# Optimization experiments

Measured on AMD Instinct MI355X. Metric: run time of the kernel, lower is better.

The kernel has to match this reference:

```python
import jax, jax.numpy as jnp
import numpy as np

N, DIM, OUT, E = 10000, 256, 256, 320000


def setup_inputs() -> dict:
    key = jax.random.key(0)
    ks = jax.random.split(key, 10)
    def w(k, shape):
        fan_in = shape[0]
        return jax.random.normal(k, shape, jnp.float32) * (fan_in ** -0.5)
    return {
        "v_c": jax.random.normal(ks[0], (N, DIM), jnp.float32),
        # row-normalized-ish random adjacency weights so A @ v stays O(1)
        "A": jax.random.uniform(ks[1], (N, N), jnp.float32) * (2.0 / N),
        "src": jax.random.randint(ks[2], (E,), 0, N, jnp.int32),
        "dst": jax.random.randint(ks[3], (E,), 0, N, jnp.int32),
        # ResidualBlock params: lin1 (dim -> 2dim), lin2 (2dim -> dim)
        "W1": w(ks[4], (DIM, 2 * DIM)), "b1": jnp.zeros((2 * DIM,), jnp.float32),
        "W2": w(ks[5], (2 * DIM, DIM)), "b2": jnp.zeros((DIM,), jnp.float32),
        # LatticeMP_Block lin1 / lin2 (dim -> out_dim)
        "Wl1": w(ks[6], (DIM, OUT)), "bl1": jnp.zeros((OUT,), jnp.float32),
        "Wl2": w(ks[7], (DIM, OUT)), "bl2": jnp.zeros((OUT,), jnp.float32),
    }


def reference(v_c, A, src, dst, W1, b1, W2, b2, Wl1, bl1, Wl2, bl2):
    # ResidualBlock: relu(h + lin2(relu(lin1(h))))
    h1 = jnp.maximum(v_c @ W1 + b1, 0.0) @ W2 + b2          # [N, DIM]
    v = jnp.maximum(v_c + h1, 0.0)                           # [N, DIM]
    # relu(lin1(v)) + relu(lin2(A @ v))
    v = jnp.maximum(v @ Wl1 + bl1, 0.0) + jnp.maximum((A @ v) @ Wl2 + bl2, 0.0)  # [N, OUT]
    # DGL update_all(copy_u, sum): h_N[d] = sum_{(s,d) in E} v[s]
    h_N = jax.ops.segment_sum(v[src], dst, num_segments=N)   # [N, OUT]
    return h_N + v
```

## Files before the change

kernel.cpp:

```cpp
#include <hip/hip_runtime.h>
#include <stdint.h>

#define NN 10000
#define DIMV 256
#define HID 512
#define NEDGE 320000
#define SPLIT 6
#define KCH 1664
#define NKT 313
#define APL 2112
#define ABUF 8448
#define BOFF 16896
#define LDSZ 49664

typedef __attribute__((ext_vector_type(8))) short bf16x8;
typedef __attribute__((ext_vector_type(4))) float f32x4;
typedef __attribute__((ext_vector_type(4))) unsigned short u16x4;
typedef __attribute__((ext_vector_type(2))) unsigned int u32x2;

__device__ __forceinline__ unsigned short f2bf(float f) {
  union { float f; unsigned int u; } c; c.f = f;
  return (unsigned short)((c.u + 0x7FFFu + ((c.u >> 16) & 1u)) >> 16);
}
__device__ __forceinline__ float bf2f(unsigned short h) {
  union { unsigned int u; float f; } c; c.u = ((unsigned int)h) << 16;
  return c.f;
}

__device__ __forceinline__ bf16x8 bzero8() {
  bf16x8 r;
#pragma unroll
  for (int i = 0; i < 8; ++i) r[i] = 0;
  return r;
}

__device__ __forceinline__ bf16x8 pack8(const float* x) {
  bf16x8 r;
#pragma unroll
  for (int i = 0; i < 8; ++i) r[i] = (short)f2bf(x[i]);
  return r;
}

__device__ __forceinline__ u32x2 cvt4v(const f32x4 a) {
  u32x2 r;
  asm("v_cvt_pk_bf16_f32 %0, %1, %2" : "=v"(r[0]) : "v"(a[0]), "v"(a[1]));
  asm("v_cvt_pk_bf16_f32 %0, %1, %2" : "=v"(r[1]) : "v"(a[2]), "v"(a[3]));
  return r;
}

typedef __attribute__((address_space(1))) unsigned int gu32;
typedef __attribute__((address_space(3))) unsigned int lu32;
__device__ __forceinline__ void glds16(const void* g, void* l) {
  __builtin_amdgcn_global_load_lds((const gu32*)g, (lu32*)l, 16, 0, 0);
}

__global__ void k_conv(const float* __restrict__ W1, const float* __restrict__ W2,
                       const float* __restrict__ Wl1, const float* __restrict__ Wl2,
                       unsigned short* __restrict__ W1T, unsigned short* __restrict__ W2T,
                       unsigned short* __restrict__ Wl1T, unsigned short* __restrict__ Wl2T,
                       unsigned short* __restrict__ vB, int* __restrict__ counts) {
  int i = blockIdx.x * 256 + threadIdx.x;
  if (i < 131072) {
    { int k = i >> 9, o = i & 511; W1T[o * 256 + k] = f2bf(W1[i]); }
    { int k = i >> 8, o = i & 255; W2T[o * 512 + k] = f2bf(W2[i]); }
    if (i < 65536) {
      int k = i >> 8, o = i & 255;
      Wl1T[o * 256 + k] = f2bf(Wl1[i]);
      Wl2T[o * 256 + k] = f2bf(Wl2[i]);
    }
    if (i < 4096) {
      int c = i >> 4, kk = 16 + (i & 15);
      int g = kk >> 3;
      int byte = c * 64 + ((g ^ ((c >> 1) & 3)) << 4) + (kk & 7) * 2;
      *(unsigned short*)((char*)vB + (size_t)312 * 16384 + byte) = 0;
    }
    if (i < NN) counts[i] = 0;
  }
}

__launch_bounds__(256, 2)
__global__ void k_mlp(const float* __restrict__ vc,
                      const unsigned short* __restrict__ W1T, const float* __restrict__ b1,
                      const unsigned short* __restrict__ W2T, const float* __restrict__ b2,
                      unsigned short* __restrict__ v_rm, unsigned short* __restrict__ vB,
                      const int* __restrict__ dst, int* __restrict__ counts) {
  if (blockIdx.x >= 313) {
    const int e0 = (blockIdx.x - 313) * 256 + threadIdx.x;
    for (int e = e0; e < NEDGE; e += 40 * 256) atomicAdd(&counts[dst[e]], 1);
    return;
  }
  __shared__ __align__(16) char sm[65536];
  const int t = threadIdx.x;
  const int lane = t & 63, wid = t >> 6;
  const int wr = wid & 1, wc = wid >> 1;
  const int r0 = blockIdx.x * 32;

  {
    const int row = t >> 3, grow = r0 + row;
#pragma unroll
    for (int q = 0; q < 4; ++q) {
      const int slot = (t & 7) * 4 + q;
      float buf[8] = {0.f, 0.f, 0.f, 0.f, 0.f, 0.f, 0.f, 0.f};
      if (grow < NN) {
        const float4 x0 = *(const float4*)(vc + (size_t)grow * DIMV + slot * 8);
        const float4 x1 = *(const float4*)(vc + (size_t)grow * DIMV + slot * 8 + 4);
        buf[0] = x0.x; buf[1] = x0.y; buf[2] = x0.z; buf[3] = x0.w;
        buf[4] = x1.x; buf[5] = x1.y; buf[6] = x1.z; buf[7] = x1.w;
      }
      *(bf16x8*)(sm + row * 512 + ((slot ^ (row & 7)) * 16)) = pack8(buf);
    }
  }

  f32x4 acc1[16];
#pragma unroll
  for (int i = 0; i < 16; ++i) acc1[i] = (f32x4){0.f, 0.f, 0.f, 0.f};

  for (int step = 0; step < 8; ++step) {
    __syncthreads();
#pragma unroll
    for (int rr = 0; rr < 2; ++rr) {
      const int c = t + rr * 256;
      const unsigned short* srcp = W1T + c * 256 + step * 32;
#pragma unroll
      for (int q = 0; q < 4; ++q) {
        bf16x8 w = *(const bf16x8*)(srcp + q * 8);
        *(bf16x8*)(sm + 16384 + c * 64 + ((q ^ ((c >> 1) & 3)) * 16)) = w;
      }
    }
    __syncthreads();
    const int arow = 16 * wr + (lane & 15);
    const int aslot = step * 4 + (lane >> 4);
    const bf16x8 af = *(const bf16x8*)(sm + arow * 512 + ((aslot ^ (arow & 7)) * 16));
#pragma unroll
    for (int ct = 0; ct < 16; ++ct) {
      const int c = 256 * wc + 16 * ct + (lane & 15);
      const bf16x8 bfr =
          *(const bf16x8*)(sm + 16384 + c * 64 + ((((lane >> 4)) ^ ((c >> 1) & 3)) * 16));
      acc1[ct] = __builtin_amdgcn_mfma_f32_16x16x32_bf16(af, bfr, acc1[ct], 0, 0, 0);
    }
  }
  __syncthreads();
#pragma unroll
  for (int ct = 0; ct < 16; ++ct) {
    const int c = 256 * wc + 16 * ct + (lane & 15);
    const float bb = b1[c];
#pragma unroll
    for (int r = 0; r < 4; ++r) {
      const int row = 16 * wr + (lane >> 4) * 4 + r;
      float v = fmaxf(acc1[ct][r] + bb, 0.f);
      const int slot = c >> 3;
      *(unsigned short*)(sm + 16384 + row * 1024 + ((slot ^ (row & 7)) * 16) + (c & 7) * 2) =
          f2bf(v);
    }
  }

  f32x4 acc2[8];
#pragma unroll
  for (int i = 0; i < 8; ++i) acc2[i] = (f32x4){0.f, 0.f, 0.f, 0.f};

  for (int step = 0; step < 16; ++step) {
    __syncthreads();
    {
      const int c = t;
      const unsigned short* srcp = W2T + c * 512 + step * 32;
#pragma unroll
      for (int q = 0; q < 4; ++q) {
        bf16x8 w = *(const bf16x8*)(srcp + q * 8);
        *(bf16x8*)(sm + 49152 + c * 64 + ((q ^ ((c >> 1) & 3)) * 16)) = w;
      }
    }
    __syncthreads();
    const int arow = 16 * wr + (lane & 15);
    const int aslot = step * 4 + (lane >> 4);
    const bf16x8 af = *(const bf16x8*)(sm + 16384 + arow * 1024 + ((aslot ^ (arow & 7)) * 16));
#pragma unroll
    for (int ct = 0; ct < 8; ++ct) {
      const int c = 128 * wc + 16 * ct + (lane & 15);
      const bf16x8 bfr =
          *(const bf16x8*)(sm + 49152 + c * 64 + ((((lane >> 4)) ^ ((c >> 1) & 3)) * 16));
      acc2[ct] = __builtin_amdgcn_mfma_f32_16x16x32_bf16(af, bfr, acc2[ct], 0, 0, 0);
    }
  }

  const int growbase = r0 + 16 * wr + (lane >> 4) * 4;
  if (growbase < NN) {
#pragma unroll
    for (int ct = 0; ct < 8; ++ct) {
      const int c = 128 * wc + 16 * ct + (lane & 15);
      const float bb = b2[c];
      u16x4 pk;
#pragma unroll
      for (int r = 0; r < 4; ++r) {
        const int grow = growbase + r;
        float v = acc2[ct][r] + bb + vc[(size_t)grow * DIMV + c];
        v = fmaxf(v, 0.f);
        const unsigned short hv = f2bf(v);
        v_rm[(size_t)grow * DIMV + c] = hv;
        pk[r] = hv;
      }
      const int tile = growbase >> 5, kk0 = growbase & 31;
      const int g = kk0 >> 3;
      const int byte = c * 64 + ((g ^ ((c >> 1) & 3)) << 4) + (kk0 & 7) * 2;
      *(u16x4*)((char*)vB + (size_t)tile * 16384 + byte) = pk;
    }
  }
}

__launch_bounds__(512, 4)
__global__ void k_av(const float* __restrict__ A, const unsigned short* __restrict__ vB,
                     unsigned short* __restrict__ avpb,
                     const int* __restrict__ counts, int* __restrict__ offsets,
                     int* __restrict__ cursor) {
  __shared__ __align__(16) char sm[LDSZ];
  const int t = threadIdx.x, lane = t & 63, wid = t >> 6;

  if (blockIdx.x >= 474) {
    int* wred = (int*)sm;
    int carry = 0;
    for (int base = 0; base < NN; base += 512) {
      const int i = base + t;
      const int x = (i < NN) ? counts[i] : 0;
      int v = x;
#pragma unroll
      for (int d = 1; d < 64; d <<= 1) {
        int y = __shfl_up(v, d);
        if (lane >= d) v += y;
      }
      if (lane == 63) wred[wid] = v;
      __syncthreads();
      if (t < 8) {
        int sv = wred[t];
#pragma unroll
        for (int d = 1; d < 8; d <<= 1) {
          int y = __shfl_up(sv, d);
          if (t >= d) sv += y;
        }
        wred[t] = sv;
      }
      __syncthreads();
      const int excl = carry + (wid ? wred[wid - 1] : 0) + v - x;
      if (i < NN) { offsets[i] = excl; cursor[i] = excl; }
      carry += wred[7];
      __syncthreads();
    }
    if (t == 0) offsets[NN] = carry;
    return;
  }

  const int wr = wid >> 2, wc = wid & 3;

  const int orig = blockIdx.x;
  const int xcd = orig & 7, idx = orig >> 3;
  const int g = (xcd < 2) ? xcd * 60 + idx : 120 + (xcd - 2) * 59 + idx;
  const int s = g / 79;
  const int xb = g - s * 79;
  const int r0 = xb * 128;
  const int kbase = s * KCH;
  const int tile0 = s * 52;
  const int nst = (s == SPLIT - 1) ? 53 : 52;
  unsigned short* outp = avpb + (size_t)s * NN * DIMV;

  const int srow = t >> 3, sQ = t & 7;
  const float* ap0 = A + (size_t)min(r0 + srow, NN - 1) * NN;
  const float* ap1 = A + (size_t)min(r0 + 64 + srow, NN - 1) * NN;
  const int wbase = (sQ >> 1) * APL + (sQ & 1) * 8;
  const int w0 = wbase + srow * 16;
  const int w1 = wbase + (64 + srow) * 16;

  f32x4 aR0, aR1, bR0, bR1;

#define AISSUE_A(ST)                                          \
  do {                                                        \
    int kq = min(kbase + (ST)*32 + sQ * 4, 9996);             \
    aR0 = *(const f32x4*)(ap0 + kq);                          \
    aR1 = *(const f32x4*)(ap1 + kq);                          \
  } while (0)
#define AISSUE_B(ST)                                          \
  do {                                                        \
    int kq = min(kbase + (ST)*32 + sQ * 4, 9996);             \
    bR0 = *(const f32x4*)(ap0 + kq);                          \
    bR1 = *(const f32x4*)(ap1 + kq);                          \
  } while (0)
#define AWRITE_A(BUF)                                         \
  do {                                                        \
    char* wb = sm + (BUF)*ABUF;                               \
    *(u32x2*)(wb + w0) = cvt4v(aR0);                          \
    *(u32x2*)(wb + w1) = cvt4v(aR1);                          \
  } while (0)
#define AWRITE_B(BUF)                                         \
  do {                                                        \
    char* wb = sm + (BUF)*ABUF;                               \
    *(u32x2*)(wb + w0) = cvt4v(bR0);                          \
    *(u32x2*)(wb + w1) = cvt4v(bR1);                          \
  } while (0)

#define BSTAGE(BUF, TILE)                                                     \
  do {                                                                        \
    char* lb = sm + BOFF + (BUF)*16384 + wid * 1024;                          \
    const char* gp = (const char*)vB + (size_t)(TILE)*16384 + wid * 1024 +    \
                     lane * 16;                                               \
    glds16(gp, lb);                                                           \
    glds16(gp + 8192, lb + 8192);                                             \
  } while (0)

  f32x4 acc[4][4];
#pragma unroll
  for (int i = 0; i < 4; ++i)
#pragma unroll
    for (int j = 0; j < 4; ++j) acc[i][j] = (f32x4){0.f, 0.f, 0.f, 0.f};

  const int rbase = (lane >> 4) * APL + (wr * 64 + (lane & 15)) * 16;
  int boff[4];
#pragma unroll
  for (int ct = 0; ct < 4; ++ct) {
    const int col = wc * 64 + ct * 16 + (lane & 15);
    boff[ct] = col * 64 + (((lane >> 4) ^ ((col >> 1) & 3)) << 4);
  }

#define COMPUTE(CUR)                                                               \
  do {                                                                            \
    const char* ab = sm + (CUR)*ABUF;                                             \
    const char* bb = sm + BOFF + (CUR)*16384;                                     \
    const bf16x8 af0 = *(const bf16x8*)(ab + rbase);                              \
    const bf16x8 af1 = *(const bf16x8*)(ab + rbase + 256);                        \
    const bf16x8 af2 = *(const bf16x8*)(ab + rbase + 512);                        \
    const bf16x8 af3 = *(const bf16x8*)(ab + rbase + 768);                        \
    _Pragma("unroll") for (int ct = 0; ct < 4; ++ct) {                            \
      const bf16x8 bfr = *(const bf16x8*)(bb + boff[ct]);                         \
      acc[0][ct] = __builtin_amdgcn_mfma_f32_16x16x32_bf16(af0, bfr, acc[0][ct], 0, 0, 0); \
      acc[1][ct] = __builtin_amdgcn_mfma_f32_16x16x32_bf16(af1, bfr, acc[1][ct], 0, 0, 0); \
      acc[2][ct] = __builtin_amdgcn_mfma_f32_16x16x32_bf16(af2, bfr, acc[2][ct], 0, 0, 0); \
      acc[3][ct] = __builtin_amdgcn_mfma_f32_16x16x32_bf16(af3, bfr, acc[3][ct], 0, 0, 0); \
    }                                                                             \
  } while (0)

  AISSUE_A(0);
  AWRITE_A(0);
  BSTAGE(0, tile0);
  AISSUE_B(1);
  __builtin_amdgcn_sched_barrier(0);
  asm volatile("s_waitcnt lgkmcnt(0)" ::: "memory");
  asm volatile("s_waitcnt vmcnt(2)" ::: "memory");
  __builtin_amdgcn_sched_barrier(0);
  __builtin_amdgcn_s_barrier();

  int cur = 0;
  for (int st = 0; st < nst; ++st) {
    const bool more = (st + 1 < nst);
    const bool more2 = (st + 2 < nst);
    if (more) BSTAGE(cur ^ 1, tile0 + st + 1);
    if (more2) {
      if ((st & 1) == 0) AISSUE_A(st + 2); else AISSUE_B(st + 2);
    }
    COMPUTE(cur);
    if (more) {
      if ((st & 1) == 0) AWRITE_B(cur ^ 1); else AWRITE_A(cur ^ 1);
    }
    __builtin_amdgcn_sched_barrier(0);
    asm volatile("s_waitcnt lgkmcnt(0)" ::: "memory");
    if (more2) asm volatile("s_waitcnt vmcnt(2)" ::: "memory");
    else       asm volatile("s_waitcnt vmcnt(0)" ::: "memory");
    __builtin_amdgcn_sched_barrier(0);
    __builtin_amdgcn_s_barrier();
    cur ^= 1;
  }
#undef AISSUE_A
#undef AISSUE_B
#undef AWRITE_A
#undef AWRITE_B
#undef BSTAGE
#undef COMPUTE

#pragma unroll
  for (int rt = 0; rt < 4; ++rt) {
    const int gb = r0 + wr * 64 + rt * 16 + (lane >> 4) * 4;
    if (gb < NN) {
#pragma unroll
      for (int ct = 0; ct < 4; ++ct) {
        const int col = wc * 64 + ct * 16 + (lane & 15);
#pragma unroll
        for (int r = 0; r < 4; ++r)
          outp[(size_t)(gb + r) * DIMV + col] = f2bf(acc[rt][ct][r]);
      }
    }
  }
}

__launch_bounds__(256, 2)
__global__ void k_out(const unsigned short* __restrict__ v_rm,
                      const unsigned short* __restrict__ avpb,
                      const unsigned short* __restrict__ Wl1T, const float* __restrict__ bl1,
                      const unsigned short* __restrict__ Wl2T, const float* __restrict__ bl2,
                      unsigned short* __restrict__ v2b, float* __restrict__ outb,
                      const int* __restrict__ src, const int* __restrict__ dst,
                      int* __restrict__ cursor, int* __restrict__ srcbuf) {
  if (blockIdx.x >= 313) {
    const int e0 = (blockIdx.x - 313) * 256 + threadIdx.x;
    for (int e = e0; e < NEDGE; e += 40 * 256) {
      const int pos = atomicAdd(&cursor[dst[e]], 1);
      srcbuf[pos] = src[e];
    }
    return;
  }
  __shared__ __align__(16) char sm[65536];
  const int t = threadIdx.x, lane = t & 63, wid = t >> 6;
  const int wr = wid & 1, wc = wid >> 1;
  const int r0 = blockIdx.x * 32;

  {
    const int row = t >> 3, grow = r0 + row;
#pragma unroll
    for (int q = 0; q < 4; ++q) {
      const int slot = (t & 7) * 4 + q;
      bf16x8 w = (grow < NN) ? *(const bf16x8*)(v_rm + (size_t)grow * DIMV + slot * 8) : bzero8();
      *(bf16x8*)(sm + row * 512 + ((slot ^ (row & 7)) * 16)) = w;
    }
#pragma unroll
    for (int q = 0; q < 4; ++q) {
      const int slot = (t & 7) * 4 + q;
      float buf[8] = {0.f, 0.f, 0.f, 0.f, 0.f, 0.f, 0.f, 0.f};
      if (grow < NN) {
#pragma unroll
        for (int p = 0; p < SPLIT; ++p) {
          const bf16x8 a =
              *(const bf16x8*)(avpb + (size_t)p * NN * DIMV + (size_t)grow * DIMV + slot * 8);
#pragma unroll
          for (int z = 0; z < 8; ++z) buf[z] += bf2f((unsigned short)a[z]);
        }
      }
      *(bf16x8*)(sm + 16384 + row * 512 + ((slot ^ (row & 7)) * 16)) = pack8(buf);
    }
  }

  f32x4 acc1[8], acc2[8];
#pragma unroll
  for (int i = 0; i < 8; ++i) {
    acc1[i] = (f32x4){0.f, 0.f, 0.f, 0.f};
    acc2[i] = (f32x4){0.f, 0.f, 0.f, 0.f};
  }

  for (int step = 0; step < 8; ++step) {
    __syncthreads();
    {
      const int c = t;
      const unsigned short* s1 = Wl1T + c * 256 + step * 32;
      const unsigned short* s2 = Wl2T + c * 256 + step * 32;
#pragma unroll
      for (int q = 0; q < 4; ++q) {
        const int ps = (q ^ ((c >> 1) & 3)) * 16;
        *(bf16x8*)(sm + 32768 + c * 64 + ps) = *(const bf16x8*)(s1 + q * 8);
        *(bf16x8*)(sm + 49152 + c * 64 + ps) = *(const bf16x8*)(s2 + q * 8);
      }
    }
    __syncthreads();
    const int arow = 16 * wr + (lane & 15);
    const int aslot = step * 4 + (lane >> 4);
    const bf16x8 a1 = *(const bf16x8*)(sm + arow * 512 + ((aslot ^ (arow & 7)) * 16));
    const bf16x8 a2 = *(const bf16x8*)(sm + 16384 + arow * 512 + ((aslot ^ (arow & 7)) * 16));
#pragma unroll
    for (int ct = 0; ct < 8; ++ct) {
      const int c = 128 * wc + 16 * ct + (lane & 15);
      const int bs = (((lane >> 4)) ^ ((c >> 1) & 3)) * 16;
      acc1[ct] = __builtin_amdgcn_mfma_f32_16x16x32_bf16(
          a1, *(const bf16x8*)(sm + 32768 + c * 64 + bs), acc1[ct], 0, 0, 0);
      acc2[ct] = __builtin_amdgcn_mfma_f32_16x16x32_bf16(
          a2, *(const bf16x8*)(sm + 49152 + c * 64 + bs), acc2[ct], 0, 0, 0);
    }
  }

  const int growbase = r0 + 16 * wr + (lane >> 4) * 4;
  if (growbase < NN) {
#pragma unroll
    for (int ct = 0; ct < 8; ++ct) {
      const int c = 128 * wc + 16 * ct + (lane & 15);
      const float u1 = bl1[c], u2 = bl2[c];
#pragma unroll
      for (int r = 0; r < 4; ++r) {
        const float x = fmaxf(acc1[ct][r] + u1, 0.f) + fmaxf(acc2[ct][r] + u2, 0.f);
        v2b[(size_t)(growbase + r) * DIMV + c] = f2bf(x);
        outb[(size_t)(growbase + r) * DIMV + c] = x;
      }
    }
  }
}

__launch_bounds__(256)
__global__ void k_gather(const unsigned short* __restrict__ v2b,
                         const int* __restrict__ offsets,
                         const int* __restrict__ srcbuf, float* __restrict__ outb) {
  const int n = (blockIdx.x * 256 + threadIdx.x) >> 6;
  if (n >= NN) return;
  const int lane = threadIdx.x & 63;
  const int beg = offsets[n], end = offsets[n + 1];
  float4 a0 = {0.f, 0.f, 0.f, 0.f}, a1 = a0, a2 = a0, a3 = a0;
  float4 a4 = a0, a5 = a0, a6 = a0, a7 = a0;
  int j = beg;
  for (; j + 8 <= end; j += 8) {
    const int s0 = srcbuf[j], s1 = srcbuf[j + 1], s2 = srcbuf[j + 2], s3 = srcbuf[j + 3];
    const int s4 = srcbuf[j + 4], s5 = srcbuf[j + 5], s6 = srcbuf[j + 6], s7 = srcbuf[j + 7];
    const u16x4 x0 = *(const u16x4*)(v2b + (size_t)s0 * DIMV + lane * 4);
    const u16x4 x1 = *(const u16x4*)(v2b + (size_t)s1 * DIMV + lane * 4);
    const u16x4 x2 = *(const u16x4*)(v2b + (size_t)s2 * DIMV + lane * 4);
    const u16x4 x3 = *(const u16x4*)(v2b + (size_t)s3 * DIMV + lane * 4);
    const u16x4 x4 = *(const u16x4*)(v2b + (size_t)s4 * DIMV + lane * 4);
    const u16x4 x5 = *(const u16x4*)(v2b + (size_t)s5 * DIMV + lane * 4);
    const u16x4 x6 = *(const u16x4*)(v2b + (size_t)s6 * DIMV + lane * 4);
    const u16x4 x7 = *(const u16x4*)(v2b + (size_t)s7 * DIMV + lane * 4);
    a0.x += bf2f(x0[0]); a0.y += bf2f(x0[1]); a0.z += bf2f(x0[2]); a0.w += bf2f(x0[3]);
    a1.x += bf2f(x1[0]); a1.y += bf2f(x1[1]); a1.z += bf2f(x1[2]); a1.w += bf2f(x1[3]);
    a2.x += bf2f(x2[0]); a2.y += bf2f(x2[1]); a2.z += bf2f(x2[2]); a2.w += bf2f(x2[3]);
    a3.x += bf2f(x3[0]); a3.y += bf2f(x3[1]); a3.z += bf2f(x3[2]); a3.w += bf2f(x3[3]);
    a4.x += bf2f(x4[0]); a4.y += bf2f(x4[1]); a4.z += bf2f(x4[2]); a4.w += bf2f(x4[3]);
    a5.x += bf2f(x5[0]); a5.y += bf2f(x5[1]); a5.z += bf2f(x5[2]); a5.w += bf2f(x5[3]);
    a6.x += bf2f(x6[0]); a6.y += bf2f(x6[1]); a6.z += bf2f(x6[2]); a6.w += bf2f(x6[3]);
    a7.x += bf2f(x7[0]); a7.y += bf2f(x7[1]); a7.z += bf2f(x7[2]); a7.w += bf2f(x7[3]);
  }
  for (; j < end; ++j) {
    const int s0 = srcbuf[j];
    const u16x4 x0 = *(const u16x4*)(v2b + (size_t)s0 * DIMV + lane * 4);
    a0.x += bf2f(x0[0]); a0.y += bf2f(x0[1]); a0.z += bf2f(x0[2]); a0.w += bf2f(x0[3]);
  }
  a0.x += a1.x + a2.x + a3.x + a4.x + a5.x + a6.x + a7.x;
  a0.y += a1.y + a2.y + a3.y + a4.y + a5.y + a6.y + a7.y;
  a0.z += a1.z + a2.z + a3.z + a4.z + a5.z + a6.z + a7.z;
  a0.w += a1.w + a2.w + a3.w + a4.w + a5.w + a6.w + a7.w;
  float* o = outb + (size_t)n * DIMV + lane * 4;
  float4 cur = *(const float4*)o;
  cur.x += a0.x; cur.y += a0.y; cur.z += a0.z; cur.w += a0.w;
  *(float4*)o = cur;
}

extern "C" void kernel_launch(void* const* d_in, const int* in_sizes, int n_in,
                              void* d_out, int out_size, void* d_ws, size_t ws_size,
                              hipStream_t stream) {
  const float* vc  = (const float*)d_in[0];
  const float* A   = (const float*)d_in[1];
  const int*   src = (const int*)d_in[2];
  const int*   dst = (const int*)d_in[3];
  const float* W1  = (const float*)d_in[4];
  const float* b1  = (const float*)d_in[5];
  const float* W2  = (const float*)d_in[6];
  const float* b2  = (const float*)d_in[7];
  const float* Wl1 = (const float*)d_in[8];
  const float* bl1 = (const float*)d_in[9];
  const float* Wl2 = (const float*)d_in[10];
  const float* bl2 = (const float*)d_in[11];
  float* outb = (float*)d_out;
  char* ws = (char*)d_ws;

  unsigned short* W1T  = (unsigned short*)(ws + 0);
  unsigned short* W2T  = (unsigned short*)(ws + 262144);
  unsigned short* Wl1T = (unsigned short*)(ws + 524288);
  unsigned short* Wl2T = (unsigned short*)(ws + 655360);
  unsigned short* vB   = (unsigned short*)(ws + 786432);
  unsigned short* v_rm = (unsigned short*)(ws + 5914624);
  int* counts  = (int*)(ws + 11034624);
  int* offsets = (int*)(ws + 11075584);
  int* cursor  = (int*)(ws + 11116544);
  int* srcbuf  = (int*)(ws + 11157504);
  unsigned short* avpb = (unsigned short*)(ws + 12437760);
  unsigned short* v2b  = (unsigned short*)(ws + 43157760);

  hipLaunchKernelGGL(k_conv, dim3(512), dim3(256), 0, stream,
                     W1, W2, Wl1, Wl2, W1T, W2T, Wl1T, Wl2T, vB, counts);
  hipLaunchKernelGGL(k_mlp, dim3(353), dim3(256), 0, stream,
                     vc, W1T, b1, W2T, b2, v_rm, vB, dst, counts);
  hipLaunchKernelGGL(k_av, dim3(475), dim3(512), 0, stream,
                     A, vB, avpb, counts, offsets, cursor);
  hipLaunchKernelGGL(k_out, dim3(353), dim3(256), 0, stream,
                     v_rm, avpb, Wl1T, bl1, Wl2T, bl2, v2b, outb,
                     src, dst, cursor, srcbuf);
  hipLaunchKernelGGL(k_gather, dim3((NN * 64 + 255) / 256), dim3(256), 0, stream,
                     v2b, offsets, srcbuf, outb);
}
```

Baseline: 239.5 us.

## Load two A K-steps per issue with 16-byte writes and pad K tiles

The A@v kernel now loads 8 floats per thread per row, covering two K-steps at once. It writes them to LDS as single 16-byte stores into a four-slot A buffer, where it previously issued 4-float loads every step. The K range is padded to 324 tiles so all six splits run an equal 54 steps, and the padding region of vB is zeroed. This halves the number of global-load issue points and evens the load across splits. In exchange it uses more LDS, about 67KB against 49KB, which may reduce occupancy, and it does extra padded work.

New measurement: 238.2 us. About the same (-0.5%).

```diff
diff --git a/kernel.cpp b/kernel.cpp
--- a/kernel.cpp
+++ b/kernel.cpp
@@ -6,17 +6,18 @@
 #define HID 512
 #define NEDGE 320000
 #define SPLIT 6
-#define KCH 1664
-#define NKT 313
-#define APL 2112
-#define ABUF 8448
-#define BOFF 16896
-#define LDSZ 49664
+#define KCH 1728
+#define NKTP 324
+#define APL 2144
+#define ABUF 8576
+#define BOFF 34304
+#define LDSZ 67072
 
 typedef __attribute__((ext_vector_type(8))) short bf16x8;
 typedef __attribute__((ext_vector_type(4))) float f32x4;
 typedef __attribute__((ext_vector_type(4))) unsigned short u16x4;
 typedef __attribute__((ext_vector_type(2))) unsigned int u32x2;
+typedef __attribute__((ext_vector_type(4))) unsigned int u32x4;
 
 __device__ __forceinline__ unsigned short f2bf(float f) {
   union { float f; unsigned int u; } c; c.f = f;
@@ -68,11 +69,8 @@
       Wl1T[o * 256 + k] = f2bf(Wl1[i]);
       Wl2T[o * 256 + k] = f2bf(Wl2[i]);
     }
-    if (i < 4096) {
-      int c = i >> 4, kk = 16 + (i & 15);
-      int g = kk >> 3;
-      int byte = c * 64 + ((g ^ ((c >> 1) & 3)) << 4) + (kk & 7) * 2;
-      *(unsigned short*)((char*)vB + (size_t)312 * 16384 + byte) = 0;
+    if (i < 49152) {
+      ((unsigned int*)vB)[1277952 + i] = 0;
     }
     if (i < NN) counts[i] = 0;
   }
@@ -256,42 +254,34 @@
   const int xb = g - s * 79;
   const int r0 = xb * 128;
   const int kbase = s * KCH;
-  const int tile0 = s * 52;
-  const int nst = (s == SPLIT - 1) ? 53 : 52;
+  const int tile0 = s * 54;
+  const int nst = 54;
   unsigned short* outp = avpb + (size_t)s * NN * DIMV;
 
   const int srow = t >> 3, sQ = t & 7;
   const float* ap0 = A + (size_t)min(r0 + srow, NN - 1) * NN;
   const float* ap1 = A + (size_t)min(r0 + 64 + srow, NN - 1) * NN;
-  const int wbase = (sQ >> 1) * APL + (sQ & 1) * 8;
-  const int w0 = wbase + srow * 16;
-  const int w1 = wbase + (64 + srow) * 16;
-
-  f32x4 aR0, aR1, bR0, bR1;
-
-#define AISSUE_A(ST)                                          \
+
+  f32x4 aR0, aR1, aR2, aR3;
+
+#define AISSUE2(ST)                                           \
   do {                                                        \
-    int kq = min(kbase + (ST)*32 + sQ * 4, 9996);             \
+    int kq = min(kbase + (ST)*32 + sQ * 8, 9992);             \
     aR0 = *(const f32x4*)(ap0 + kq);                          \
-    aR1 = *(const f32x4*)(ap1 + kq);                          \
+    aR1 = *(const f32x4*)(ap0 + kq + 4);                      \
+    aR2 = *(const f32x4*)(ap1 + kq);                          \
+    aR3 = *(const f32x4*)(ap1 + kq + 4);                      \
   } while (0)
-#define AISSUE_B(ST)                                          \
+
+#define AWRITE2(PJ)                                           \
   do {                                                        \
-    int kq = min(kbase + (ST)*32 + sQ * 4, 9996);             \
-    bR0 = *(const f32x4*)(ap0 + kq);                          \
-    bR1 = *(const f32x4*)(ap1 + kq);                          \
-  } while (0)
-#define AWRITE_A(BUF)                                         \
-  do {                                                        \
-    char* wb = sm + (BUF)*ABUF;                               \
-    *(u32x2*)(wb + w0) = cvt4v(aR0);                          \
-    *(u32x2*)(wb + w1) = cvt4v(aR1);                          \
-  } while (0)
-#define AWRITE_B(BUF)                                         \
-  do {                                                        \
-    char* wb = sm + (BUF)*ABUF;                               \
-    *(u32x2*)(wb + w0) = cvt4v(bR0);                          \
-    *(u32x2*)(wb + w1) = cvt4v(bR1);                          \
+    char* base_ = sm + (2 * (PJ) + (sQ >> 2)) * ABUF + (sQ & 3) * APL; \
+    u32x2 lo_ = cvt4v(aR0), hi_ = cvt4v(aR1);                 \
+    u32x4 w0_ = {lo_[0], lo_[1], hi_[0], hi_[1]};             \
+    *(u32x4*)(base_ + srow * 16) = w0_;                       \
+    lo_ = cvt4v(aR2); hi_ = cvt4v(aR3);                       \
+    u32x4 w1_ = {lo_[0], lo_[1], hi_[0], hi_[1]};             \
+    *(u32x4*)(base_ + (64 + srow) * 16) = w1_;                \
   } while (0)
 
 #define BSTAGE(BUF, TILE)                                                     \
@@ -317,9 +307,9 @@
     boff[ct] = col * 64 + (((lane >> 4) ^ ((col >> 1) & 3)) << 4);
   }
 
-#define COMPUTE(CUR)                                                               \
+#define COMPUTE(ST, CUR)                                                           \
   do {                                                                            \
-    const char* ab = sm + (CUR)*ABUF;                                             \
+    const char* ab = sm + (2 * (((ST) >> 1) & 1) + ((ST)&1)) * ABUF;              \
     const char* bb = sm + BOFF + (CUR)*16384;                                     \
     const bf16x8 af0 = *(const bf16x8*)(ab + rbase);                              \
     const bf16x8 af1 = *(const bf16x8*)(ab + rbase + 256);                        \
@@ -334,40 +324,33 @@
     }                                                                             \
   } while (0)
 
-  AISSUE_A(0);
-  AWRITE_A(0);
+  AISSUE2(0);
   BSTAGE(0, tile0);
-  AISSUE_B(1);
+  AWRITE2(0);
   __builtin_amdgcn_sched_barrier(0);
   asm volatile("s_waitcnt lgkmcnt(0)" ::: "memory");
-  asm volatile("s_waitcnt vmcnt(2)" ::: "memory");
+  asm volatile("s_waitcnt vmcnt(0)" ::: "memory");
   __builtin_amdgcn_sched_barrier(0);
   __builtin_amdgcn_s_barrier();
 
   int cur = 0;
   for (int st = 0; st < nst; ++st) {
     const bool more = (st + 1 < nst);
-    const bool more2 = (st + 2 < nst);
+    const bool issueA = ((st & 1) == 0) && (st + 2 < nst);
     if (more) BSTAGE(cur ^ 1, tile0 + st + 1);
-    if (more2) {
-      if ((st & 1) == 0) AISSUE_A(st + 2); else AISSUE_B(st + 2);
-    }
-    COMPUTE(cur);
-    if (more) {
-      if ((st & 1) == 0) AWRITE_B(cur ^ 1); else AWRITE_A(cur ^ 1);
-    }
+    if (issueA) AISSUE2(st + 2);
+    COMPUTE(st, cur);
+    if ((st & 1) == 1 && more) AWRITE2(((st + 1) >> 1) & 1);
     __builtin_amdgcn_sched_barrier(0);
     asm volatile("s_waitcnt lgkmcnt(0)" ::: "memory");
-    if (more2) asm volatile("s_waitcnt vmcnt(2)" ::: "memory");
-    else       asm volatile("s_waitcnt vmcnt(0)" ::: "memory");
+    if (issueA) asm volatile("s_waitcnt vmcnt(4)" ::: "memory");
+    else        asm volatile("s_waitcnt vmcnt(0)" ::: "memory");
     __builtin_amdgcn_sched_barrier(0);
     __builtin_amdgcn_s_barrier();
     cur ^= 1;
   }
-#undef AISSUE_A
-#undef AISSUE_B
-#undef AWRITE_A
-#undef AWRITE_B
+#undef AISSUE2
+#undef AWRITE2
 #undef BSTAGE
 #undef COMPUTE
 
@@ -553,13 +536,13 @@
   unsigned short* Wl1T = (unsigned short*)(ws + 524288);
   unsigned short* Wl2T = (unsigned short*)(ws + 655360);
   unsigned short* vB   = (unsigned short*)(ws + 786432);
-  unsigned short* v_rm = (unsigned short*)(ws + 5914624);
-  int* counts  = (int*)(ws + 11034624);
-  int* offsets = (int*)(ws + 11075584);
-  int* cursor  = (int*)(ws + 11116544);
-  int* srcbuf  = (int*)(ws + 11157504);
-  unsigned short* avpb = (unsigned short*)(ws + 12437760);
-  unsigned short* v2b  = (unsigned short*)(ws + 43157760);
+  unsigned short* v_rm = (unsigned short*)(ws + 6094848);
+  int* counts  = (int*)(ws + 11214848);
+  int* offsets = (int*)(ws + 11255808);
+  int* cursor  = (int*)(ws + 11296768);
+  int* srcbuf  = (int*)(ws + 11337728);
+  unsigned short* avpb = (unsigned short*)(ws + 12617728);
+  unsigned short* v2b  = (unsigned short*)(ws + 43337728);
 
   hipLaunchKernelGGL(k_conv, dim3(512), dim3(256), 0, stream,
                      W1, W2, Wl1, Wl2, W1T, W2T, Wl1T, Wl2T, vB, counts);
```
